# Kernel optimization log

Measured on AMD Instinct MI355X. Metric: run time of the kernel, lower is better.

Reference implementation:

```python
import jax, jax.numpy as jnp
import numpy as np

WINDOW = 5  # len_sort_window in the original module


def setup_inputs() -> dict:
    key = jax.random.key(0)
    k1, k2, k3 = jax.random.split(key, 3)
    B, L, D = 8, 4000, 512  # L divisible by WINDOW, D < L
    q = jax.random.normal(k1, (B, L, D), dtype=jnp.float32)
    k = jax.random.normal(k2, (B, L, D), dtype=jnp.float32)
    v = jax.random.normal(k3, (B, L, D), dtype=jnp.float32)
    return {"q": q, "k": k, "v": v}


def reference(q, k, v):
    # q, k are unused by the original forward.
    B, L, D = v.shape
    t = jnp.arange(L)          # sequence positions
    s = jnp.arange(D)          # per-feature cyclic shift amount (= feature index)
    # Shift feature i left by i: shifted[:, t, i] = v[:, (t + i) % L, i]
    idx_fwd = (t[:, None] + s[None, :]) % L            # [L, D]
    v_shift = jnp.take_along_axis(v, idx_fwd[None, :, :], axis=1)  # [B, L, D]
    # Sort within fixed non-overlapping windows of size WINDOW along the seq axis.
    v_sorted = jnp.sort(v_shift.reshape(B, L // WINDOW, WINDOW, D), axis=2)
    v_sorted = v_sorted.reshape(B, L, D)
    # Unshift feature i right by i: out[:, t, i] = v_sorted[:, (t - i) % L, i]
    idx_bwd = (t[:, None] - s[None, :]) % L            # [L, D]
    return jnp.take_along_axis(v_sorted, idx_bwd[None, :, :], axis=1)
```

## Files before the change

kernel.cpp:

```cpp
#include <hip/hip_runtime.h>


constexpr int L = 4000;
constexpr int D = 512;

__global__ __launch_bounds__(256)
void swd18_window_sort(const float* __restrict__ v, float* __restrict__ out) {
    const int i = blockIdx.y * 256 + threadIdx.x;
    const int w = blockIdx.x;
    const int b = blockIdx.z;

    const int r = i % 5;
    const int s = w * 5 + r;

    const float* __restrict__ vb = v + (size_t)b * (size_t)(L * D);
    float*       __restrict__ ob = out + (size_t)b * (size_t)(L * D);

    int t0 = s;
    int t1 = s + 1; if (t1 >= L) t1 -= L;
    int t2 = s + 2; if (t2 >= L) t2 -= L;
    int t3 = s + 3; if (t3 >= L) t3 -= L;
    int t4 = s + 4; if (t4 >= L) t4 -= L;

    float x0 = vb[t0 * D + i];
    float x1 = vb[t1 * D + i];
    float x2 = vb[t2 * D + i];
    float x3 = vb[t3 * D + i];
    float x4 = vb[t4 * D + i];

#define CE(a, b) { float lo_ = fminf(a, b); float hi_ = fmaxf(a, b); a = lo_; b = hi_; }
    CE(x0, x1) CE(x3, x4) CE(x2, x4) CE(x2, x3) CE(x1, x4)
    CE(x0, x3) CE(x0, x2) CE(x1, x3) CE(x1, x2)
#undef CE

    ob[t0 * D + i] = x0;
    ob[t1 * D + i] = x1;
    ob[t2 * D + i] = x2;
    ob[t3 * D + i] = x3;
    ob[t4 * D + i] = x4;
}

extern "C" void kernel_launch(void* const* d_in, const int* in_sizes, int n_in,
                              void* d_out, int out_size, void* d_ws, size_t ws_size,
                              hipStream_t stream) {
    const float* v = (const float*)d_in[2];
    float* out = (float*)d_out;

    const int B = in_sizes[2] / (L * D);

    dim3 grid(L / 5, D / 256, B);
    swd18_window_sort<<<grid, dim3(256), 0, stream>>>(v, out);
}
```

Baseline: 193.7 us.

## Write each output row group once via 15-row window reload and XCD-aware block mapping

```diff
diff --git a/kernel.cpp b/kernel.cpp
--- a/kernel.cpp
+++ b/kernel.cpp
@@ -1,44 +1,72 @@
 #include <hip/hip_runtime.h>
 
 
-constexpr int L = 4000;
-constexpr int D = 512;
+constexpr int L  = 4000;
+constexpr int D  = 512;
+constexpr int NG = L / 5;
+constexpr int GCHUNK = NG / 8;
+
+#define CE(a, b) { float lo_ = fminf(a, b); float hi_ = fmaxf(a, b); (a) = lo_; (b) = hi_; }
 
 __global__ __launch_bounds__(256)
-void swd18_window_sort(const float* __restrict__ v, float* __restrict__ out) {
-    const int i = blockIdx.y * 256 + threadIdx.x;
-    const int w = blockIdx.x;
-    const int b = blockIdx.z;
+void swd18_col(const float* __restrict__ v, float* __restrict__ out) {
+    const int lin  = blockIdx.x;
+    const int xcd  = lin & 7;
+    const int seq  = lin >> 3;
+    const int b    = seq / (2 * GCHUNK);
+    const int rest = seq % (2 * GCHUNK);
+    const int gin  = rest >> 1;
+    const int half = rest & 1;
+    const int g    = xcd * GCHUNK + gin;
 
-    const int r = i % 5;
-    const int s = w * 5 + r;
+    const int i = half * 256 + threadIdx.x;
 
-    const float* __restrict__ vb = v + (size_t)b * (size_t)(L * D);
-    float*       __restrict__ ob = out + (size_t)b * (size_t)(L * D);
+    const float* __restrict__ vb = v   + (size_t)b * (L * D);
+    float*       __restrict__ ob = out + (size_t)b * (L * D);
 
-    int t0 = s;
-    int t1 = s + 1; if (t1 >= L) t1 -= L;
-    int t2 = s + 2; if (t2 >= L) t2 -= L;
-    int t3 = s + 3; if (t3 >= L) t3 -= L;
-    int t4 = s + 4; if (t4 >= L) t4 -= L;
+    float r[15];
+#pragma unroll
+    for (int j = 0; j < 15; ++j) {
+        int row = 5 * g - 5 + j;
+        if (row < 0)  row += L;
+        if (row >= L) row -= L;
+        r[j] = vb[(size_t)row * D + i];
+    }
 
-    float x0 = vb[t0 * D + i];
-    float x1 = vb[t1 * D + i];
-    float x2 = vb[t2 * D + i];
-    float x3 = vb[t3 * D + i];
-    float x4 = vb[t4 * D + i];
+    const int rc = i % 5;
+    const bool e0 = rc == 0, e1 = rc == 1, e2 = rc == 2, e3 = rc == 3;
 
-#define CE(a, b) { float lo_ = fminf(a, b); float hi_ = fmaxf(a, b); a = lo_; b = hi_; }
-    CE(x0, x1) CE(x3, x4) CE(x2, x4) CE(x2, x3) CE(x1, x4)
-    CE(x0, x3) CE(x0, x2) CE(x1, x3) CE(x1, x2)
+    float A0 = e0 ? r[0] : e1 ? r[1] : e2 ? r[2] : e3 ? r[3] : r[4];
+    float A1 = e0 ? r[1] : e1 ? r[2] : e2 ? r[3] : e3 ? r[4] : r[5];
+    float A2 = e0 ? r[2] : e1 ? r[3] : e2 ? r[4] : e3 ? r[5] : r[6];
+    float A3 = e0 ? r[3] : e1 ? r[4] : e2 ? r[5] : e3 ? r[6] : r[7];
+    float A4 = e0 ? r[4] : e1 ? r[5] : e2 ? r[6] : e3 ? r[7] : r[8];
+    float B0 = e0 ? r[5] : e1 ? r[6] : e2 ? r[7] : e3 ? r[8] : r[9];
+    float B1 = e0 ? r[6] : e1 ? r[7] : e2 ? r[8] : e3 ? r[9] : r[10];
+    float B2 = e0 ? r[7] : e1 ? r[8] : e2 ? r[9] : e3 ? r[10] : r[11];
+    float B3 = e0 ? r[8] : e1 ? r[9] : e2 ? r[10] : e3 ? r[11] : r[12];
+    float B4 = e0 ? r[9] : e1 ? r[10] : e2 ? r[11] : e3 ? r[12] : r[13];
+
+    CE(A0, A1) CE(A3, A4) CE(A2, A4) CE(A2, A3) CE(A1, A4)
+    CE(A0, A3) CE(A0, A2) CE(A1, A3) CE(A1, A2)
+    CE(B0, B1) CE(B3, B4) CE(B2, B4) CE(B2, B3) CE(B1, B4)
+    CE(B0, B3) CE(B0, B2) CE(B1, B3) CE(B1, B2)
+
+    float f0 = e0 ? B0 : e1 ? A4 : e2 ? A3 : e3 ? A2 : A1;
+    float f1 = e0 ? B1 : e1 ? B0 : e2 ? A4 : e3 ? A3 : A2;
+    float f2 = e0 ? B2 : e1 ? B1 : e2 ? B0 : e3 ? A4 : A3;
+    float f3 = e0 ? B3 : e1 ? B2 : e2 ? B1 : e3 ? B0 : A4;
+    float f4 = e0 ? B4 : e1 ? B3 : e2 ? B2 : e3 ? B1 : B0;
+
+    float* o = ob + (size_t)(5 * g) * D + i;
+    __builtin_nontemporal_store(f0, o + 0 * D);
+    __builtin_nontemporal_store(f1, o + 1 * D);
+    __builtin_nontemporal_store(f2, o + 2 * D);
+    __builtin_nontemporal_store(f3, o + 3 * D);
+    __builtin_nontemporal_store(f4, o + 4 * D);
+}
+
 #undef CE
-
-    ob[t0 * D + i] = x0;
-    ob[t1 * D + i] = x1;
-    ob[t2 * D + i] = x2;
-    ob[t3 * D + i] = x3;
-    ob[t4 * D + i] = x4;
-}
 
 extern "C" void kernel_launch(void* const* d_in, const int* in_sizes, int n_in,
                               void* d_out, int out_size, void* d_ws, size_t ws_size,
@@ -47,7 +75,6 @@
     float* out = (float*)d_out;
 
     const int B = in_sizes[2] / (L * D);
-
-    dim3 grid(L / 5, D / 256, B);
-    swd18_window_sort<<<grid, dim3(256), 0, stream>>>(v, out);
+    const int nblocks = B * NG * 2;
+    swd18_col<<<dim3(nblocks), dim3(256), 0, stream>>>(v, out);
 }
```

Result: faster. 179.0 us (-7.6%).
